# Kernel tuning notes

Hardware: AMD Instinct MI355X
Metric: run time of the kernel (lower is better)

## Reference

```python
import jax, jax.numpy as jnp
import numpy as np

H = 5  # hidden size (hardcoded in the torch module)


def setup_inputs() -> dict:
    key = jax.random.key(0)
    ks = jax.random.split(key, 9)
    N, T = 32768, 600
    s = 1.0 / np.sqrt(H)  # torch LSTM/Linear init scale (uniform bound), use as stddev
    return {
        "x": jax.random.normal(ks[0], (N, T), dtype=jnp.float32),
        "w_ih": jax.random.normal(ks[1], (4 * H, 1), dtype=jnp.float32) * s,
        "w_hh": jax.random.normal(ks[2], (4 * H, H), dtype=jnp.float32) * s,
        "b_ih": jax.random.normal(ks[3], (4 * H,), dtype=jnp.float32) * s,
        "b_hh": jax.random.normal(ks[4], (4 * H,), dtype=jnp.float32) * s,
        "fc_w": jax.random.normal(ks[5], (15, H), dtype=jnp.float32) * s,
        "fc_b": jax.random.normal(ks[6], (15,), dtype=jnp.float32) * s,
        "out_w": jax.random.normal(ks[7], (1, 15), dtype=jnp.float32) * (1.0 / np.sqrt(15)),
        "out_b": jax.random.normal(ks[8], (1,), dtype=jnp.float32) * (1.0 / np.sqrt(15)),
    }


def reference(x, w_ih, w_hh, b_ih, b_hh, fc_w, fc_b, out_w, out_b):
    # x: (N, T) -> unsqueeze to feature dim of 1 is implicit (input_size=1).
    N = x.shape[0]
    b = b_ih + b_hh  # (4H,)
    w_ih_vec = w_ih[:, 0]  # (4H,) since input_size == 1

    def step(carry, x_t):
        h, c = carry  # (N, H) each
        # gates: (N, 4H); PyTorch gate order: i, f, g, o
        gates = x_t[:, None] * w_ih_vec + h @ w_hh.T + b
        i = jax.nn.sigmoid(gates[:, 0 * H:1 * H])
        f = jax.nn.sigmoid(gates[:, 1 * H:2 * H])
        g = jnp.tanh(gates[:, 2 * H:3 * H])
        o = jax.nn.sigmoid(gates[:, 3 * H:4 * H])
        c = f * c + i * g
        h = o * jnp.tanh(c)
        return (h, c), None

    h0 = jnp.zeros((N, H), dtype=x.dtype)
    c0 = jnp.zeros((N, H), dtype=x.dtype)
    (h_T, _), _ = jax.lax.scan(step, (h0, c0), x.T)  # scan over time: xs (T, N)
    # Head: only the last timestep's hidden state is used.
    hid = h_T @ fc_w.T + fc_b          # (N, 15)
    out = hid @ out_w.T + out_b        # (N, 1)
    return jax.nn.sigmoid(out)
```

## Files before the change

### kernel.cpp

```cpp
#include <hip/hip_runtime.h>
#include <math.h>


#define LOG2E 1.44269504088896340736f

typedef float v2f __attribute__((ext_vector_type(2)));

constexpr int T_ = 600;
constexpr int SEQ_PER_BLOCK = 32;
constexpr int TTILE = 64;
constexpr int NTILES = (T_ + TTILE - 1) / TTILE;
constexpr int LDS_STRIDE = 68;
constexpr int XBUF = SEQ_PER_BLOCK * LDS_STRIDE;

__device__ __forceinline__ float fast_rcp(float v)  { return __builtin_amdgcn_rcpf(v); }
__device__ __forceinline__ float fast_exp2(float v) { return __builtin_amdgcn_exp2f(v); }

template <int CTRL>
__device__ __forceinline__ float dpp_q(float v) {
    const int x = __float_as_int(v);
    return __int_as_float(__builtin_amdgcn_update_dpp(x, x, CTRL, 0xF, 0xF, false));
}

__global__ __launch_bounds__(64, 1) void lstm_kernel(
    const float* __restrict__ x,
    const float* __restrict__ w_ih,
    const float* __restrict__ w_hh,
    const float* __restrict__ b_ih,
    const float* __restrict__ b_hh,
    const float* __restrict__ fc_w,
    const float* __restrict__ fc_b,
    const float* __restrict__ out_w,
    const float* __restrict__ out_b,
    float* __restrict__ out)
{
    __shared__ float xs[2 * XBUF];

    const int lane = threadIdx.x;
    const int s    = lane >> 1;
    const int half = lane & 1;
    const int seq  = blockIdx.x * SEQ_PER_BLOCK + s;

    const int rloT[2][5] = {{0, 1, 2, 5, 6}, {3, 4, 7, 8, 9}};
    const int rhiT[2][5] = {{10, 11, 12, 15, 16}, {13, 14, 17, 18, 19}};
    const int gtT [2][5] = {{1, 1, 1, 0, 0}, {1, 1, 0, 0, 0}};

    v2f wih2[5], bb2[5], whh2[5][5];
#pragma unroll
    for (int p = 0; p < 5; ++p) {
        const int rlo = rloT[half][p], rhi = rhiT[half][p];
        const float sl = -LOG2E;
        const float sh = gtT[half][p] ? (-2.0f * LOG2E) : (-LOG2E);
        wih2[p] = (v2f){ w_ih[rlo] * sl, w_ih[rhi] * sh };
        bb2[p]  = (v2f){ (b_ih[rlo] + b_hh[rlo]) * sl,
                         (b_ih[rhi] + b_hh[rhi]) * sh };
#pragma unroll
        for (int k = 0; k < 5; ++k)
            whh2[p][k] = (v2f){ w_hh[rlo * 5 + k] * sl, w_hh[rhi * 5 + k] * sh };
    }
    const int ng = half ? 2 : 3;

    float H[5] = {0.f, 0.f, 0.f, 0.f, 0.f};
    float cA = 0.f, cB = 0.f, cC = 0.f;

    const float* xblk = x + (size_t)(blockIdx.x * SEQ_PER_BLOCK) * T_;

    auto step = [&](float xt) {
        const v2f x2 = (v2f){ xt, xt };
        v2f g2[5];
#pragma unroll
        for (int p = 0; p < 5; ++p) g2[p] = x2 * wih2[p] + bb2[p];
#pragma unroll
        for (int k = 0; k < 5; ++k) {
            const v2f h2 = (v2f){ H[k], H[k] };
#pragma unroll
            for (int p = 0; p < 5; ++p) g2[p] += h2 * whh2[p][k];
        }
        v2f act2[5];
#pragma unroll
        for (int p = 0; p < 5; ++p) {
            const float dx = 1.0f + fast_exp2(g2[p].x);
            const float dy = 1.0f + fast_exp2(g2[p].y);
            const float rp = fast_rcp(dx * dy);
            act2[p].x = rp * dy;
            act2[p].y = rp * dx;
        }
#pragma unroll
        for (int p = 0; p < 3; ++p)
            if (p < ng)
                act2[p].y = fmaf(act2[p].y, -4.0f * LOG2E, 2.0f * LOG2E);
        const float PA = act2[0].x * act2[0].y;
        const float PB = act2[1].x * act2[1].y;
        const float P2 = dpp_q<0xA0>(act2[2].x * act2[2].y);
        const float f2 = dpp_q<0xF5>(act2[2].x);
        const float o2 = dpp_q<0xF5>(act2[2].y);
        cA = fmaf(act2[3].x, cA, PA);
        cB = fmaf(act2[4].x, cB, PB);
        cC = fmaf(f2, cC, P2);
        const float dA = 1.0f + fast_exp2(cA);
        const float dB = 1.0f + fast_exp2(cB);
        const float dC = 1.0f + fast_exp2(cC);
        const float q  = fast_rcp(dA * dB);
        const float tA = fmaf(q * dB, 2.0f, -1.0f);
        const float tB = fmaf(q * dA, 2.0f, -1.0f);
        const float tC = fmaf(fast_rcp(dC), 2.0f, -1.0f);
        const float hA = act2[3].y * tA;
        const float hB = act2[4].y * tB;
        H[0] = dpp_q<0xA0>(hA);
        H[1] = dpp_q<0xA0>(hB);
        H[2] = o2 * tC;
        H[3] = dpp_q<0xF5>(hA);
        H[4] = dpp_q<0xF5>(hB);
    };

    const int rrow = lane >> 4;
    const int ccol = (lane & 15) << 2;

#pragma unroll
    for (int it = 0; it < 8; ++it) {
        const int r = it * 4 + rrow;
        const float4 v = *(const float4*)(xblk + (size_t)r * T_ + ccol);
        *(float4*)&xs[r * LDS_STRIDE + ccol] = v;
    }
    __syncthreads();

    for (int tile = 0; tile < NTILES; ++tile) {
        const int tpf  = (tile + 1 < NTILES) ? (tile + 1) : (NTILES - 1);
        const int cpf  = (tpf * TTILE + ccol <= T_ - 4) ? (tpf * TTILE + ccol) : (T_ - 4);
        float4 pf[8];
#pragma unroll
        for (int it = 0; it < 8; ++it) {
            const int r = it * 4 + rrow;
            pf[it] = *(const float4*)(xblk + (size_t)r * T_ + cpf);
        }
        const int t0i   = tile * TTILE;
        const int steps = (T_ - t0i >= TTILE) ? TTILE : (T_ - t0i);
        const float* xr = &xs[(tile & 1) * XBUF + s * LDS_STRIDE];
        float4 cur = *(const float4*)&xr[0];
        for (int tt = 0; tt < steps; tt += 4) {
            const float4 nxt = *(const float4*)&xr[tt + 4];
            step(cur.x);
            step(cur.y);
            step(cur.z);
            step(cur.w);
            cur = nxt;
        }
        float* xw = &xs[((tile + 1) & 1) * XBUF];
#pragma unroll
        for (int it = 0; it < 8; ++it) {
            const int r = it * 4 + rrow;
            *(float4*)&xw[r * LDS_STRIDE + ccol] = pf[it];
        }
        __syncthreads();
    }

    if (half == 0) {
        float acc = out_b[0];
#pragma unroll
        for (int j = 0; j < 15; ++j) {
            float hid = fc_b[j];
#pragma unroll
            for (int k = 0; k < 5; ++k) hid = fmaf(H[k], fc_w[j * 5 + k], hid);
            acc = fmaf(hid, out_w[j], acc);
        }
        out[seq] = fast_rcp(1.0f + fast_exp2(-acc * LOG2E));
    }
}

extern "C" void kernel_launch(void* const* d_in, const int* in_sizes, int n_in,
                              void* d_out, int out_size, void* d_ws, size_t ws_size,
                              hipStream_t stream) {
    const float* x    = (const float*)d_in[0];
    const float* w_ih = (const float*)d_in[1];
    const float* w_hh = (const float*)d_in[2];
    const float* b_ih = (const float*)d_in[3];
    const float* b_hh = (const float*)d_in[4];
    const float* fc_w = (const float*)d_in[5];
    const float* fc_b = (const float*)d_in[6];
    const float* out_w = (const float*)d_in[7];
    const float* out_b = (const float*)d_in[8];
    float* out = (float*)d_out;

    const int N = in_sizes[0] / T_;
    const int grid = N / SEQ_PER_BLOCK;
    hipLaunchKernelGGL(lstm_kernel, dim3(grid), dim3(64), 0, stream,
                       x, w_ih, w_hh, b_ih, b_hh, fc_w, fc_b, out_w, out_b, out);
}
```

Before: 248.4 us.

## Split each LSTM sequence across four lanes instead of two

Each sequence is now handled by a quad of four lanes rather than a pair. Each lane computes gates for one hidden unit, and the fifth unit's four gates are spread across the quad. Results are broadcast with quad DPP. This shortens each lane's per-step serial dependency chain at the cost of twice as many waves and 16 sequences per block, with launch bounds raised to allow two waves per SIMD. It also adds some redundant work for the fifth hidden unit and more x tile loads per sequence.

```diff
diff --git a/kernel.cpp b/kernel.cpp
--- a/kernel.cpp
+++ b/kernel.cpp
@@ -7,7 +7,7 @@
 typedef float v2f __attribute__((ext_vector_type(2)));
 
 constexpr int T_ = 600;
-constexpr int SEQ_PER_BLOCK = 32;
+constexpr int SEQ_PER_BLOCK = 16;
 constexpr int TTILE = 64;
 constexpr int NTILES = (T_ + TTILE - 1) / TTILE;
 constexpr int LDS_STRIDE = 68;
@@ -22,7 +22,7 @@
     return __int_as_float(__builtin_amdgcn_update_dpp(x, x, CTRL, 0xF, 0xF, false));
 }
 
-__global__ __launch_bounds__(64, 1) void lstm_kernel(
+__global__ __launch_bounds__(64, 2) void lstm_kernel(
     const float* __restrict__ x,
     const float* __restrict__ w_ih,
     const float* __restrict__ w_hh,
@@ -37,87 +37,93 @@
     __shared__ float xs[2 * XBUF];
 
     const int lane = threadIdx.x;
-    const int s    = lane >> 1;
-    const int half = lane & 1;
-    const int seq  = blockIdx.x * SEQ_PER_BLOCK + s;
+    const int s    = lane >> 2;
+    const int l    = lane & 3;
 
-    const int rloT[2][5] = {{0, 1, 2, 5, 6}, {3, 4, 7, 8, 9}};
-    const int rhiT[2][5] = {{10, 11, 12, 15, 16}, {13, 14, 17, 18, 19}};
-    const int gtT [2][5] = {{1, 1, 1, 0, 0}, {1, 1, 0, 0, 0}};
+    const int rA0 = l;
+    const int rA1 = 10 + l;
+    const int rB0 = 5 + l;
+    const int rB1 = 15 + l;
+    const int rE  = 4 + 5 * l;
+    const float sSig = -LOG2E;
+    const float sTan = -2.0f * LOG2E;
+    const float sE   = (l == 2) ? sTan : sSig;
 
-    v2f wih2[5], bb2[5], whh2[5][5];
+    v2f wihA, wihB, bbA, bbB, whhA[5], whhB[5];
+    float wihE, bbE, whhE[5];
+    {
+        wihA = (v2f){ w_ih[rA0] * sSig, w_ih[rA1] * sTan };
+        wihB = (v2f){ w_ih[rB0] * sSig, w_ih[rB1] * sSig };
+        wihE = w_ih[rE] * sE;
+        bbA  = (v2f){ (b_ih[rA0] + b_hh[rA0]) * sSig,
+                      (b_ih[rA1] + b_hh[rA1]) * sTan };
+        bbB  = (v2f){ (b_ih[rB0] + b_hh[rB0]) * sSig,
+                      (b_ih[rB1] + b_hh[rB1]) * sSig };
+        bbE  = (b_ih[rE] + b_hh[rE]) * sE;
 #pragma unroll
-    for (int p = 0; p < 5; ++p) {
-        const int rlo = rloT[half][p], rhi = rhiT[half][p];
-        const float sl = -LOG2E;
-        const float sh = gtT[half][p] ? (-2.0f * LOG2E) : (-LOG2E);
-        wih2[p] = (v2f){ w_ih[rlo] * sl, w_ih[rhi] * sh };
-        bb2[p]  = (v2f){ (b_ih[rlo] + b_hh[rlo]) * sl,
-                         (b_ih[rhi] + b_hh[rhi]) * sh };
-#pragma unroll
-        for (int k = 0; k < 5; ++k)
-            whh2[p][k] = (v2f){ w_hh[rlo * 5 + k] * sl, w_hh[rhi * 5 + k] * sh };
+        for (int k = 0; k < 5; ++k) {
+            whhA[k] = (v2f){ w_hh[rA0 * 5 + k] * sSig, w_hh[rA1 * 5 + k] * sTan };
+            whhB[k] = (v2f){ w_hh[rB0 * 5 + k] * sSig, w_hh[rB1 * 5 + k] * sSig };
+            whhE[k] = w_hh[rE * 5 + k] * sE;
+        }
     }
-    const int ng = half ? 2 : 3;
 
     float H[5] = {0.f, 0.f, 0.f, 0.f, 0.f};
-    float cA = 0.f, cB = 0.f, cC = 0.f;
+    float cL = 0.f;
+    float c4 = 0.f;
 
     const float* xblk = x + (size_t)(blockIdx.x * SEQ_PER_BLOCK) * T_;
 
     auto step = [&](float xt) {
         const v2f x2 = (v2f){ xt, xt };
-        v2f g2[5];
-#pragma unroll
-        for (int p = 0; p < 5; ++p) g2[p] = x2 * wih2[p] + bb2[p];
+        v2f gA = x2 * wihA + bbA;
+        v2f gB = x2 * wihB + bbB;
+        float gE = fmaf(xt, wihE, bbE);
 #pragma unroll
         for (int k = 0; k < 5; ++k) {
             const v2f h2 = (v2f){ H[k], H[k] };
-#pragma unroll
-            for (int p = 0; p < 5; ++p) g2[p] += h2 * whh2[p][k];
+            gA += h2 * whhA[k];
+            gB += h2 * whhB[k];
+            gE  = fmaf(H[k], whhE[k], gE);
         }
-        v2f act2[5];
-#pragma unroll
-        for (int p = 0; p < 5; ++p) {
-            const float dx = 1.0f + fast_exp2(g2[p].x);
-            const float dy = 1.0f + fast_exp2(g2[p].y);
-            const float rp = fast_rcp(dx * dy);
-            act2[p].x = rp * dy;
-            act2[p].y = rp * dx;
-        }
-#pragma unroll
-        for (int p = 0; p < 3; ++p)
-            if (p < ng)
-                act2[p].y = fmaf(act2[p].y, -4.0f * LOG2E, 2.0f * LOG2E);
-        const float PA = act2[0].x * act2[0].y;
-        const float PB = act2[1].x * act2[1].y;
-        const float P2 = dpp_q<0xA0>(act2[2].x * act2[2].y);
-        const float f2 = dpp_q<0xF5>(act2[2].x);
-        const float o2 = dpp_q<0xF5>(act2[2].y);
-        cA = fmaf(act2[3].x, cA, PA);
-        cB = fmaf(act2[4].x, cB, PB);
-        cC = fmaf(f2, cC, P2);
-        const float dA = 1.0f + fast_exp2(cA);
-        const float dB = 1.0f + fast_exp2(cB);
-        const float dC = 1.0f + fast_exp2(cC);
-        const float q  = fast_rcp(dA * dB);
-        const float tA = fmaf(q * dB, 2.0f, -1.0f);
-        const float tB = fmaf(q * dA, 2.0f, -1.0f);
-        const float tC = fmaf(fast_rcp(dC), 2.0f, -1.0f);
-        const float hA = act2[3].y * tA;
-        const float hB = act2[4].y * tB;
-        H[0] = dpp_q<0xA0>(hA);
-        H[1] = dpp_q<0xA0>(hB);
-        H[2] = o2 * tC;
-        H[3] = dpp_q<0xF5>(hA);
-        H[4] = dpp_q<0xF5>(hB);
+        const float dAx = 1.0f + fast_exp2(gA.x);
+        const float dAy = 1.0f + fast_exp2(gA.y);
+        const float dBx = 1.0f + fast_exp2(gB.x);
+        const float dBy = 1.0f + fast_exp2(gB.y);
+        const float dE  = 1.0f + fast_exp2(gE);
+        const float rpA = fast_rcp(dAx * dAy);
+        const float mB  = dBx * dBy;
+        const float rp3 = fast_rcp(mB * dE);
+        const float i_l = rpA * dAy;
+        const float gt  = fmaf(rpA * dAx, -4.0f * LOG2E, 2.0f * LOG2E);
+        const float f_l = rp3 * (dBy * dE);
+        const float o_l = rp3 * (dBx * dE);
+        const float vE  = rp3 * mB;
+        const float vEg = fmaf(vE, -4.0f * LOG2E, 2.0f * LOG2E);
+        const float i4 = dpp_q<0x00>(vE);
+        const float f4 = dpp_q<0x55>(vE);
+        const float g4 = dpp_q<0xAA>(vEg);
+        const float o4 = dpp_q<0xFF>(vE);
+        cL = fmaf(f_l, cL, i_l * gt);
+        c4 = fmaf(f4, c4, i4 * g4);
+        const float dL = 1.0f + fast_exp2(cL);
+        const float d4 = 1.0f + fast_exp2(c4);
+        const float q  = fast_rcp(dL * d4);
+        const float tL = fmaf(q * d4, 2.0f, -1.0f);
+        const float t4 = fmaf(q * dL, 2.0f, -1.0f);
+        const float hL = o_l * tL;
+        H[4] = o4 * t4;
+        H[0] = dpp_q<0x00>(hL);
+        H[1] = dpp_q<0x55>(hL);
+        H[2] = dpp_q<0xAA>(hL);
+        H[3] = dpp_q<0xFF>(hL);
     };
 
     const int rrow = lane >> 4;
     const int ccol = (lane & 15) << 2;
 
 #pragma unroll
-    for (int it = 0; it < 8; ++it) {
+    for (int it = 0; it < 4; ++it) {
         const int r = it * 4 + rrow;
         const float4 v = *(const float4*)(xblk + (size_t)r * T_ + ccol);
         *(float4*)&xs[r * LDS_STRIDE + ccol] = v;
@@ -125,11 +131,11 @@
     __syncthreads();
 
     for (int tile = 0; tile < NTILES; ++tile) {
-        const int tpf  = (tile + 1 < NTILES) ? (tile + 1) : (NTILES - 1);
-        const int cpf  = (tpf * TTILE + ccol <= T_ - 4) ? (tpf * TTILE + ccol) : (T_ - 4);
-        float4 pf[8];
+        const int tpf = (tile + 1 < NTILES) ? (tile + 1) : (NTILES - 1);
+        const int cpf = (tpf * TTILE + ccol <= T_ - 4) ? (tpf * TTILE + ccol) : (T_ - 4);
+        float4 pf[4];
 #pragma unroll
-        for (int it = 0; it < 8; ++it) {
+        for (int it = 0; it < 4; ++it) {
             const int r = it * 4 + rrow;
             pf[it] = *(const float4*)(xblk + (size_t)r * T_ + cpf);
         }
@@ -147,14 +153,14 @@
         }
         float* xw = &xs[((tile + 1) & 1) * XBUF];
 #pragma unroll
-        for (int it = 0; it < 8; ++it) {
+        for (int it = 0; it < 4; ++it) {
             const int r = it * 4 + rrow;
             *(float4*)&xw[r * LDS_STRIDE + ccol] = pf[it];
         }
         __syncthreads();
     }
 
-    if (half == 0) {
+    if (l == 0) {
         float acc = out_b[0];
 #pragma unroll
         for (int j = 0; j < 15; ++j) {
@@ -163,7 +169,7 @@
             for (int k = 0; k < 5; ++k) hid = fmaf(H[k], fc_w[j * 5 + k], hid);
             acc = fmaf(hid, out_w[j], acc);
         }
-        out[seq] = fast_rcp(1.0f + fast_exp2(-acc * LOG2E));
+        out[blockIdx.x * SEQ_PER_BLOCK + s] = fast_rcp(1.0f + fast_exp2(-acc * LOG2E));
     }
 }
 
```

Result: slower. 275.0 us (+10.7%).
